# Optimization experiments

Measured on AMD Instinct MI355X. Metric: run time of the kernel, lower is better.

Reference implementation:

```python
import jax, jax.numpy as jnp
import numpy as np

B, F, SF = 2, 5, 15          # batch, query frames, num_shots*sframe
C, KD, VD = 1024, 128, 512   # encoder_dim, keydim, valdim
H = W = 32                   # l3 feature map (output stride 8 on 256x256)


def _conv(x, w, b, pad):
    y = jax.lax.conv_general_dilated(
        x, w, window_strides=(1, 1), padding=[(pad, pad), (pad, pad)],
        dimension_numbers=("NCHW", "OIHW", "NCHW"))
    return y + b[None, :, None, None]


def setup_inputs() -> dict:
    key = jax.random.key(0)
    ks = jax.random.split(key, 8)
    s = 0.02
    return {
        "query_feat": jax.random.normal(ks[0], (B * F, C, H, W), jnp.float32),
        "support_fg_feat": jax.random.normal(ks[1], (B * SF, C, H, W), jnp.float32),
        "w_sk": jax.random.normal(ks[2], (KD, C, 3, 3), jnp.float32) * s,
        "b_sk": jnp.zeros((KD,), jnp.float32),
        "w_sv": jax.random.normal(ks[3], (VD, C, 3, 3), jnp.float32) * s,
        "b_sv": jnp.zeros((VD,), jnp.float32),
        "w_qq": jax.random.normal(ks[4], (KD, C, 3, 3), jnp.float32) * s,
        "b_qq": jnp.zeros((KD,), jnp.float32),
        "w_qk": jax.random.normal(ks[5], (KD, C, 3, 3), jnp.float32) * s,
        "b_qk": jnp.zeros((KD,), jnp.float32),
        "w_cq": jax.random.normal(ks[6], (VD, C, 1, 1), jnp.float32) * s,
        "b_cq": jnp.zeros((VD,), jnp.float32),
    }


def reference(query_feat, support_fg_feat, w_sk, b_sk, w_sv, b_sv,
              w_qq, b_qq, w_qk, b_qk, w_cq, b_cq):
    hw = H * W
    # QKV projections (3x3 convs)
    sk = _conv(support_fg_feat, w_sk, b_sk, 1)   # [B*SF, KD, H, W]
    sv = _conv(support_fg_feat, w_sv, b_sv, 1)   # [B*SF, VD, H, W]
    qq = _conv(query_feat, w_qq, b_qq, 1)        # [B*F, KD, H, W]
    qk = _conv(query_feat, w_qk, b_qk, 1)        # [B*F, KD, H, W]

    # support K: [B, SF*hw, KD];  support V: [B, VD, SF*hw]
    support_k = sk.reshape(B, SF, KD, H, W).transpose(0, 2, 1, 3, 4)
    support_k = support_k.reshape(B, KD, SF * hw).transpose(0, 2, 1)
    support_v = sv.reshape(B, SF, VD, H, W).transpose(0, 2, 1, 3, 4)
    support_v = support_v.reshape(B, VD, SF * hw)

    qq5 = qq.reshape(B, F, KD, H, W)
    qk5 = qk.reshape(B, F, KD, H, W)
    mid = F // 2
    scale = 1.0 / jnp.sqrt(jnp.float32(KD))

    # stage 1: middle-frame query attends into support memory
    middle_q = qq5[:, mid].reshape(B, KD, hw)                 # [B, KD, hw]
    P1 = jnp.einsum("bkc,bcq->bkq", support_k, middle_q) * scale  # [B, SF*hw, hw]
    P1 = jax.nn.softmax(P1, axis=1)
    new_V = jnp.einsum("bvk,bkq->bvq", support_v, P1)          # [B, VD, hw]

    # stage 2: all-frame queries attend into middle-frame keys
    middle_K = qk5[:, mid].reshape(B, KD, hw).transpose(0, 2, 1)   # [B, hw, KD]
    qq_flat = qq5.transpose(0, 2, 1, 3, 4).reshape(B, KD, F * hw)  # [B, KD, F*hw]
    P2 = jnp.einsum("bkc,bcq->bkq", middle_K, qq_flat) * scale     # [B, hw, F*hw]
    P2 = jax.nn.softmax(P2, axis=1)
    Out = jnp.einsum("bvk,bkq->bvq", new_V, P2)                    # [B, VD, F*hw]

    after = Out.reshape(B, VD, F, H, W).transpose(0, 2, 1, 3, 4)
    after = after.reshape(B * F, VD, H, W)
    qf = _conv(query_feat, w_cq, b_cq, 0)                          # [B*F, VD, H, W]
    return jnp.concatenate([after, qf], axis=1)                    # [B*F, 2*VD, H, W]
```

## Files before the change

### kernel.cpp

```cpp
#include <hip/hip_runtime.h>
#include <cstdint>

typedef unsigned short u16;
typedef __attribute__((ext_vector_type(8))) u16 u16x8;
typedef __attribute__((ext_vector_type(4))) u16 u16x4;
typedef __attribute__((ext_vector_type(8))) _Float16 f16x8;
typedef __attribute__((ext_vector_type(4))) float f32x4;

__device__ __forceinline__ u16 f2h(float f) {
  _Float16 h = (_Float16)f;
  return __builtin_bit_cast(u16, h);
}
__device__ __forceinline__ float h2f(u16 b) {
  _Float16 h = __builtin_bit_cast(_Float16, b);
  return (float)h;
}
__device__ __forceinline__ void gll16(const void* g, void* l) {
  auto gp = reinterpret_cast<const __attribute__((address_space(1))) unsigned int*>(
      reinterpret_cast<uintptr_t>(g));
  auto lp = reinterpret_cast<__attribute__((address_space(3))) unsigned int*>(
      reinterpret_cast<uintptr_t>(l));
  __builtin_amdgcn_global_load_lds(gp, lp, 16, 0, 0);
}

__global__ __launch_bounds__(256) void pad_nhwc(const float* __restrict__ in,
                                                u16* __restrict__ outp) {
  const int img = blockIdx.x >> 5;
  const int y   = blockIdx.x & 31;
  __shared__ float tile[32][33];
  const int tid = threadIdx.x;
  u16* base = outp + (long)img * 34 * 34 * 1024;
  const u16x8 z8 = {0, 0, 0, 0, 0, 0, 0, 0};
  {
    u16* r = base + (long)(y + 1) * 34 * 1024;
    if (tid < 128) *(u16x8*)&r[tid * 8] = z8;
    else *(u16x8*)&r[33 * 1024 + (tid - 128) * 8] = z8;
  }
  if (y == 0) {
    for (int i = tid * 8; i < 34816; i += 2048) *(u16x8*)&base[i] = z8;
  }
  if (y == 31) {
    u16* r = base + 33L * 34 * 1024;
    for (int i = tid * 8; i < 34816; i += 2048) *(u16x8*)&r[i] = z8;
  }
  const int xi = tid & 31, ci = tid >> 5;
  const int xo = tid >> 3, q = tid & 7;
  const float* ip = in + (long)img * 1048576 + y * 32;
  u16* op = base + ((long)(y + 1) * 34 + 1) * 1024;
  for (int c0 = 0; c0 < 1024; c0 += 32) {
#pragma unroll
    for (int k2 = 0; k2 < 4; k2++)
      tile[k2 * 8 + ci][xi] = ip[(long)(c0 + k2 * 8 + ci) * 1024 + xi];
    __syncthreads();
    u16x4 o4;
#pragma unroll
    for (int r = 0; r < 4; r++) o4[r] = f2h(tile[q * 4 + r][xo]);
    *(u16x4*)&op[(long)xo * 1024 + c0 + q * 4] = o4;
    __syncthreads();
  }
}

__device__ __forceinline__ void wre3_body(const float* __restrict__ wp,
                                          u16* __restrict__ op, float* buf) {
  for (int i = threadIdx.x; i < 9216; i += 256) buf[i] = wp[i];
  __syncthreads();
  for (int k = threadIdx.x; k < 9216; k += 256) {
    const int cblk = k / 576;
    const int r = k - cblk * 576;
    const int t = r >> 6, ci = r & 63;
    op[k] = f2h(buf[(cblk * 64 + ci) * 9 + t]);
  }
}
__global__ __launch_bounds__(256) void wprep(
    const float* __restrict__ w_sk, const float* __restrict__ w_sv,
    const float* __restrict__ w_qq, const float* __restrict__ w_qk,
    const float* __restrict__ w_cq, u16* __restrict__ WTSK,
    u16* __restrict__ WTSV, u16* __restrict__ WTQQK, u16* __restrict__ WCQ) {
  __shared__ float buf[9216];
  const int b = blockIdx.x;
  if (b < 128) {
    wre3_body(w_sk + (long)b * 9216, WTSK + (long)b * 9216, buf);
  } else if (b < 640) {
    const int oc = b - 128;
    wre3_body(w_sv + (long)oc * 9216, WTSV + (long)oc * 9216, buf);
  } else if (b < 768) {
    const int oc = b - 640;
    wre3_body(w_qq + (long)oc * 9216, WTQQK + (long)oc * 9216, buf);
  } else if (b < 896) {
    const int oc = b - 768;
    wre3_body(w_qk + (long)oc * 9216, WTQQK + (long)(oc + 128) * 9216, buf);
  } else {
    const int i = (b - 896) * 1024 + threadIdx.x * 4;
#pragma unroll
    for (int r = 0; r < 4; r++) WCQ[i + r] = f2h(w_cq[i + r]);
  }
}

__global__ __launch_bounds__(256) void row_softmax60(u16* __restrict__ P) {
  u16* p = P + (long)blockIdx.x * 15360;
  const int tid = threadIdx.x;
  __shared__ float rm[4], rs[4];
  u16x4 v[15];
#pragma unroll
  for (int j = 0; j < 15; j++)
    v[j] = *(const u16x4*)(p + ((tid + (j << 8)) << 2));
  float m = -3.0e38f;
#pragma unroll
  for (int j = 0; j < 15; j++)
#pragma unroll
    for (int e = 0; e < 4; e++) m = fmaxf(m, h2f(v[j][e]));
#pragma unroll
  for (int o = 32; o > 0; o >>= 1) m = fmaxf(m, __shfl_xor(m, o, 64));
  if ((tid & 63) == 0) rm[tid >> 6] = m;
  __syncthreads();
  const float M = fmaxf(fmaxf(rm[0], rm[1]), fmaxf(rm[2], rm[3]));
  float s = 0.f;
#pragma unroll
  for (int j = 0; j < 15; j++)
#pragma unroll
    for (int e = 0; e < 4; e++) s += __expf(h2f(v[j][e]) - M);
#pragma unroll
  for (int o = 32; o > 0; o >>= 1) s += __shfl_xor(s, o, 64);
  if ((tid & 63) == 0) rs[tid >> 6] = s;
  __syncthreads();
  const float inv = 1.0f / (rs[0] + rs[1] + rs[2] + rs[3]);
#pragma unroll
  for (int j = 0; j < 15; j++) {
    u16x4 o4;
#pragma unroll
    for (int e = 0; e < 4; e++) o4[e] = f2h(__expf(h2f(v[j][e]) - M) * inv);
    *(u16x4*)(p + ((tid + (j << 8)) << 2)) = o4;
  }
}

__global__ __launch_bounds__(256) void row_softmax4(u16* __restrict__ P) {
  u16* p = P + (long)blockIdx.x * 1024;
  const int tid = threadIdx.x;
  __shared__ float rm[4], rs[4];
  u16x4 v = *(const u16x4*)(p + (tid << 2));
  float m = fmaxf(fmaxf(h2f(v[0]), h2f(v[1])), fmaxf(h2f(v[2]), h2f(v[3])));
#pragma unroll
  for (int o = 32; o > 0; o >>= 1) m = fmaxf(m, __shfl_xor(m, o, 64));
  if ((tid & 63) == 0) rm[tid >> 6] = m;
  __syncthreads();
  const float M = fmaxf(fmaxf(rm[0], rm[1]), fmaxf(rm[2], rm[3]));
  float s = 0.f;
#pragma unroll
  for (int e = 0; e < 4; e++) s += __expf(h2f(v[e]) - M);
#pragma unroll
  for (int o = 32; o > 0; o >>= 1) s += __shfl_xor(s, o, 64);
  if ((tid & 63) == 0) rs[tid >> 6] = s;
  __syncthreads();
  const float inv = 1.0f / (rs[0] + rs[1] + rs[2] + rs[3]);
  u16x4 o4;
#pragma unroll
  for (int e = 0; e < 4; e++) o4[e] = f2h(__expf(h2f(v[e]) - M) * inv);
  *(u16x4*)(p + (tid << 2)) = o4;
}

__global__ __launch_bounds__(256) void reduce8h(const u16* __restrict__ part,
                                                u16* __restrict__ o) {
  long j = ((long)blockIdx.x * 256 + threadIdx.x) * 4;
  int b = (int)(j >> 19);
  long i = j & 524287;
  const u16* p = part + (long)b * 4194304 + i;
  float s0 = 0.f, s1 = 0.f, s2 = 0.f, s3 = 0.f;
#pragma unroll
  for (int c = 0; c < 8; c++) {
    u16x4 v = *(const u16x4*)&p[(long)c * 524288];
    s0 += h2f(v[0]); s1 += h2f(v[1]); s2 += h2f(v[2]); s3 += h2f(v[3]);
  }
  u16x4 o4 = {f2h(s0), f2h(s1), f2h(s2), f2h(s3)};
  *(u16x4*)&o[j] = o4;
}
__global__ __launch_bounds__(256) void reduce_sk(const float* __restrict__ part,
                                                 const float* __restrict__ bias,
                                                 u16* __restrict__ o) {
  long i = ((long)blockIdx.x * 256 + threadIdx.x) * 4;
  f32x4 s = *(const f32x4*)&part[i];
  s = s + *(const f32x4*)&part[i + 3932160];
  f32x4 bb = *(const f32x4*)&bias[(int)(i & 127)];
  u16x4 o4;
#pragma unroll
  for (int r = 0; r < 4; r++) o4[r] = f2h(s[r] + bb[r]);
  *(u16x4*)&o[i] = o4;
}
__global__ __launch_bounds__(256) void reduce_qqk(
    const float* __restrict__ part, const float* __restrict__ b_qq,
    const float* __restrict__ b_qk, u16* __restrict__ QQR,
    u16* __restrict__ QKR) {
  long i = ((long)blockIdx.x * 256 + threadIdx.x) * 4;
  const int n = (int)(i >> 8), m = (int)(i & 255);
  f32x4 s = *(const f32x4*)&part[i];
  s = s + *(const f32x4*)&part[i + 2621440];
  const int lo = (m < 128);
  const int mm = m & 127;
  const float* bs = lo ? b_qq : b_qk;
  f32x4 bb = *(const f32x4*)&bs[mm];
  u16* dst = (lo ? QQR : QKR) + (long)n * 128 + mm;
  u16x4 o4;
#pragma unroll
  for (int r = 0; r < 4; r++) o4[r] = f2h(s[r] + bb[r]);
  *(u16x4*)dst = o4;
}

__global__ __launch_bounds__(512, 1)
void gemm256(const u16* __restrict__ A, const u16* __restrict__ B,
             const float* __restrict__ bias, u16* __restrict__ out) {
  __shared__ u16 lds[81920];
  const int tid = threadIdx.x, lane = tid & 63, wave = tid >> 6;
  const int nwg = gridDim.x * gridDim.y;
  int wg = blockIdx.x + gridDim.x * blockIdx.y;
  wg = (wg & 7) * (nwg >> 3) + (wg >> 3);
  const int ntile = wg % gridDim.x;
  const int mtile = wg / gridDim.x;

  const int slog = (lane & 7) ^ ((lane >> 3) & 7);
  const u16* aS[4];
  const u16* bS[4];
  int aD[4], bD[4];
#pragma unroll
  for (int j = 0; j < 4; j++) {
    const int r = wave * 32 + j * 8 + (lane >> 3);
    aS[j] = A + (long)(mtile * 256 + r) * 9216 + slog * 8;
    aD[j] = (wave * 32 + j * 8) * 64;
    const int n = ntile * 256 + r;
    const int img = n >> 10, p = n & 1023;
    const int y = p >> 5, x = p & 31;
    bS[j] = B + ((long)((img * 34 + y) * 34 + x)) * 1024 + slog * 8;
    bD[j] = (wave * 32 + j * 8) * 64;
  }

  const int g = lane >> 4, l15 = lane & 15;
  const int wm = wave >> 2, wn = wave & 3;
  int aRow[8], bRow[4], sx[2];
#pragma unroll
  for (int mi = 0; mi < 8; mi++) aRow[mi] = (wm * 128 + mi * 16 + l15) * 64;
#pragma unroll
  for (int ni = 0; ni < 4; ni++) bRow[ni] = (wn * 64 + ni * 16 + l15) * 64;
#pragma unroll
  for (int ks = 0; ks < 2; ks++) sx[ks] = ((ks * 4 + g) ^ (l15 & 7)) * 8;

  auto conv_badd = [](int kt) {
    const int cblk = kt / 9;
    const int t = kt - cblk * 9;
    const int dy = t / 3, dx = t - dy * 3;
    return (dy * 34 + dx) * 1024 + cblk * 64;
  };

  f32x4 acc[8][4];
  const f32x4 zero = {0.f, 0.f, 0.f, 0.f};
#pragma unroll
  for (int i = 0; i < 8; i++)
#pragma unroll
    for (int j = 0; j < 4; j++) acc[i][j] = zero;

  const int nkt = 144;
  {
#pragma unroll
    for (int j = 0; j < 4; j++) gll16(aS[j], &lds[aD[j]]);
    const int b0 = conv_badd(0), b1 = conv_badd(1);
#pragma unroll
    for (int j = 0; j < 4; j++) gll16(bS[j] + b0, &lds[32768 + bD[j]]);
#pragma unroll
    for (int j = 0; j < 4; j++) gll16(bS[j] + b1, &lds[49152 + bD[j]]);
    asm volatile("s_waitcnt vmcnt(4)" ::: "memory");
    __builtin_amdgcn_s_barrier();
  }

  int bc = 0;
  for (int kt = 0; kt < nkt; ++kt) {
    const int abuf = (kt & 1) << 14;
    const int anbuf = abuf ^ 16384;
    const int bbuf = 32768 + bc * 16384;
    int bsn = bc + 2; if (bsn >= 3) bsn -= 3;
    const int bnbuf = 32768 + bsn * 16384;
    const bool stA = (kt + 1 < nkt);
    const bool stB = (kt + 2 < nkt);
    const int kA = (kt + 1) << 6;
    const int bAdd2 = stB ? conv_badd(kt + 2) : 0;
    f16x8 afr[4], bfr[4];
#pragma unroll
    for (int mi = 0; mi < 4; mi++) afr[mi] = *(const f16x8*)&lds[abuf + aRow[mi] + sx[0]];
#pragma unroll
    for (int ni = 0; ni < 4; ni++) bfr[ni] = *(const f16x8*)&lds[bbuf + bRow[ni] + sx[0]];
    if (stA) {
      gll16(aS[0] + kA, &lds[anbuf + aD[0]]);
      gll16(aS[1] + kA, &lds[anbuf + aD[1]]);
    }
    __builtin_amdgcn_s_barrier();
    __builtin_amdgcn_s_setprio(1);
#pragma unroll
    for (int mi = 0; mi < 4; mi++)
#pragma unroll
      for (int ni = 0; ni < 4; ni++)
        acc[mi][ni] = __builtin_amdgcn_mfma_f32_16x16x32_f16(afr[mi], bfr[ni], acc[mi][ni], 0, 0, 0);
    __builtin_amdgcn_s_setprio(0);
    __builtin_amdgcn_s_barrier();
#pragma unroll
    for (int mi = 0; mi < 4; mi++) afr[mi] = *(const f16x8*)&lds[abuf + aRow[mi + 4] + sx[0]];
    if (stA) {
      gll16(aS[2] + kA, &lds[anbuf + aD[2]]);
      gll16(aS[3] + kA, &lds[anbuf + aD[3]]);
    }
    __builtin_amdgcn_s_barrier();
    __builtin_amdgcn_s_setprio(1);
#pragma unroll
    for (int mi = 0; mi < 4; mi++)
#pragma unroll
      for (int ni = 0; ni < 4; ni++)
        acc[mi + 4][ni] = __builtin_amdgcn_mfma_f32_16x16x32_f16(afr[mi], bfr[ni], acc[mi + 4][ni], 0, 0, 0);
    __builtin_amdgcn_s_setprio(0);
    __builtin_amdgcn_s_barrier();
#pragma unroll
    for (int mi = 0; mi < 4; mi++) afr[mi] = *(const f16x8*)&lds[abuf + aRow[mi] + sx[1]];
#pragma unroll
    for (int ni = 0; ni < 4; ni++) bfr[ni] = *(const f16x8*)&lds[bbuf + bRow[ni] + sx[1]];
    if (stB) {
      gll16(bS[0] + bAdd2, &lds[bnbuf + bD[0]]);
      gll16(bS[1] + bAdd2, &lds[bnbuf + bD[1]]);
    }
    __builtin_amdgcn_s_barrier();
    __builtin_amdgcn_s_setprio(1);
#pragma unroll
    for (int mi = 0; mi < 4; mi++)
#pragma unroll
      for (int ni = 0; ni < 4; ni++)
        acc[mi][ni] = __builtin_amdgcn_mfma_f32_16x16x32_f16(afr[mi], bfr[ni], acc[mi][ni], 0, 0, 0);
    __builtin_amdgcn_s_setprio(0);
    __builtin_amdgcn_s_barrier();
#pragma unroll
    for (int mi = 0; mi < 4; mi++) afr[mi] = *(const f16x8*)&lds[abuf + aRow[mi + 4] + sx[1]];
    if (stB) {
      gll16(bS[2] + bAdd2, &lds[bnbuf + bD[2]]);
      gll16(bS[3] + bAdd2, &lds[bnbuf + bD[3]]);
    }
    __builtin_amdgcn_s_barrier();
    __builtin_amdgcn_s_setprio(1);
#pragma unroll
    for (int mi = 0; mi < 4; mi++)
#pragma unroll
      for (int ni = 0; ni < 4; ni++)
        acc[mi + 4][ni] = __builtin_amdgcn_mfma_f32_16x16x32_f16(afr[mi], bfr[ni], acc[mi + 4][ni], 0, 0, 0);
    __builtin_amdgcn_s_setprio(0);
    if (stB) {
      asm volatile("s_waitcnt vmcnt(4)" ::: "memory");
    } else if (stA) {
      asm volatile("s_waitcnt vmcnt(0)" ::: "memory");
    }
    __builtin_amdgcn_s_barrier();
    bc = bc + 1; if (bc >= 3) bc -= 3;
  }

#pragma unroll
  for (int mi = 0; mi < 8; mi++) {
#pragma unroll
    for (int ni = 0; ni < 4; ni++) {
      f32x4 v = acc[mi][ni];
      const int m0 = mtile * 256 + wm * 128 + mi * 16 + g * 4;
      const int n = ntile * 256 + wn * 64 + ni * 16 + l15;
      const int b = (n >= 15360) ? 1 : 0;
      const int rem = n - b * 15360;
#pragma unroll
      for (int r = 0; r < 4; r++) {
        const int m = m0 + r;
        out[(long)b * 7864320 + (long)m * 15360 + rem] = f2h(v[r] + bias[m]);
      }
    }
  }
}

template <int BMODE, int EPI, int SPLITK>
__global__ __launch_bounds__(256, 2)
void gemm_nt(const u16* __restrict__ A, long Azoff, int Astride,
             const u16* __restrict__ B, long Bzoff, int Bstride,
             int K, float scale,
             const float* __restrict__ bias, const float* __restrict__ bias2,
             void* __restrict__ out0, void* __restrict__ out1,
             long out_zoff, int ldo) {
  __shared__ u16 lds[4 * 8192];
  const int tid = threadIdx.x;
  const int lane = tid & 63;
  const int wave = tid >> 6;
  const int mtile = blockIdx.y, ntile = blockIdx.x, z = blockIdx.z;

  const int zb = (SPLITK > 1) ? z / SPLITK : z;
  const int zc = (SPLITK > 1) ? z % SPLITK : 0;
  const u16* Ab = A + (long)zb * Azoff + (long)zc * K;
  const u16* Bb = B + (long)zb * Bzoff + ((BMODE == 0) ? (long)zc * K : 0);

  const int r8 = lane >> 3;
  const int sphys = lane & 7;
  const u16* aSrc[4];
  const u16* bSrc[4];
  u16* aDst[4];
  u16* bDst[4];
#pragma unroll
  for (int i = 0; i < 4; i++) {
    const int row = wave * 32 + i * 8 + r8;
    const int slog = sphys ^ (row & 7);
    aSrc[i] = Ab + (long)(mtile * 128 + row) * Astride + slog * 8;
    if (BMODE == 0) {
      bSrc[i] = Bb + (long)(ntile * 128 + row) * Bstride + slog * 8;
    } else {
      const int n = ntile * 128 + row;
      const int img = n >> 10;
      const int p = n & 1023;
      const int y = p >> 5, x = p & 31;
      bSrc[i] = Bb + ((long)(img * 34 + y) * 34 + x) * 1024 + slog * 8;
    }
    aDst[i] = &lds[0] + (wave * 32 + i * 8) * 64;
    bDst[i] = &lds[0] + 8192 + (wave * 32 + i * 8) * 64;
  }

  const int g = lane >> 4, l15 = lane & 15;
  const int wm = wave >> 1, wn = wave & 1;
  int offA[2][4], offB[2][4];
#pragma unroll
  for (int ks = 0; ks < 2; ks++) {
    const int sl = ks * 4 + g;
#pragma unroll
    for (int i = 0; i < 4; i++) {
      const int ra = wm * 64 + i * 16 + l15;
      offA[ks][i] = ra * 64 + ((sl ^ (ra & 7)) * 8);
      const int rb = wn * 64 + i * 16 + l15;
      offB[ks][i] = 8192 + rb * 64 + ((sl ^ (rb & 7)) * 8);
    }
  }

  auto stage = [&](int buf, int kb) {
    int bAdd;
    if (BMODE == 0) {
      bAdd = kb;
    } else if (BMODE == 1) {
      const int ktg = (zc * K + kb) >> 6;
      const int cblk = ktg / 9;
      const int t = ktg - cblk * 9;
      const int dy = t / 3, dx = t - dy * 3;
      bAdd = (dy * 34 + dx) * 1024 + cblk * 64;
    } else {
      bAdd = 35 * 1024 + kb;
    }
    const int bufo = buf * 16384;
#pragma unroll
    for (int i = 0; i < 4; i++) gll16(aSrc[i] + kb, aDst[i] + bufo);
#pragma unroll
    for (int i = 0; i < 4; i++) gll16(bSrc[i] + bAdd, bDst[i] + bufo);
  };

  f32x4 acc[4][4];
  const f32x4 zero = {0.f, 0.f, 0.f, 0.f};
#pragma unroll
  for (int i = 0; i < 4; i++)
#pragma unroll
    for (int j = 0; j < 4; j++) acc[i][j] = zero;

  const int nkt = K >> 6;
  stage(0, 0);
  __syncthreads();
  for (int kt = 0; kt < nkt; ++kt) {
    const int buf = kt & 1;
    if (kt + 1 < nkt) stage(buf ^ 1, (kt + 1) << 6);
#pragma unroll
    for (int ks = 0; ks < 2; ks++) {
      f16x8 af[4], bfg[4];
#pragma unroll
      for (int i = 0; i < 4; i++)
        af[i] = *(const f16x8*)&lds[buf * 16384 + offA[ks][i]];
#pragma unroll
      for (int i = 0; i < 4; i++)
        bfg[i] = *(const f16x8*)&lds[buf * 16384 + offB[ks][i]];
#pragma unroll
      for (int mi = 0; mi < 4; mi++)
#pragma unroll
        for (int ni = 0; ni < 4; ni++)
          acc[mi][ni] = __builtin_amdgcn_mfma_f32_16x16x32_f16(
              af[mi], bfg[ni], acc[mi][ni], 0, 0, 0);
    }
    __syncthreads();
  }

#pragma unroll
  for (int mi = 0; mi < 4; mi++) {
#pragma unroll
    for (int ni = 0; ni < 4; ni++) {
      f32x4 v = acc[mi][ni];
      const int m0 = mtile * 128 + wm * 64 + mi * 16 + g * 4;
      const int n = ntile * 128 + wn * 64 + ni * 16 + l15;
      if (EPI == 0) {
        u16* ob = (u16*)out0;
        const float* bs = bias;
        int mm = m0;
        if (out1 != nullptr && m0 >= 128) { ob = (u16*)out1; bs = bias2; mm = m0 - 128; }
        u16x4 pk;
#pragma unroll
        for (int r = 0; r < 4; r++) {
          float val = v[r] * scale + (bs ? bs[mm + r] : 0.f);
          pk[r] = f2h(val);
        }
        *(u16x4*)&ob[(long)n * ldo + mm] = pk;
      } else if (EPI == 1) {
        u16* ob = (u16*)out0 + (long)z * out_zoff;
#pragma unroll
        for (int r = 0; r < 4; r++) {
          const int m = m0 + r;
          float val = v[r] * scale + (bias ? bias[m] : 0.f);
          ob[(long)m * ldo + n] = f2h(val);
        }
      } else if (EPI == 2) {
        float* of = (float*)out0;
        const int img = n >> 10, p = n & 1023;
#pragma unroll
        for (int r = 0; r < 4; r++) {
          const int m = m0 + r;
          of[(long)img * 1048576 + (long)(512 + m) * 1024 + p] =
              v[r] + (bias ? bias[m] : 0.f);
        }
      } else if (EPI == 3) {
        float* of = (float*)out0;
        const int f = n >> 10, p = n & 1023;
#pragma unroll
        for (int r = 0; r < 4; r++) {
          const int m = m0 + r;
          of[(long)z * 5242880 + (long)f * 1048576 + (long)m * 1024 + p] = v[r];
        }
      } else if (EPI == 4) {
        float* of = (float*)out0 + (long)z * out_zoff;
#pragma unroll
        for (int r = 0; r < 4; r++) of[(long)(m0 + r) * ldo + n] = v[r];
      } else if (EPI == 5) {
        float* of = (float*)out0 + (long)zc * out_zoff;
        *(f32x4*)&of[(long)n * ldo + m0] = v;
      } else {
        u16* ob = (u16*)out0 + (long)z * out_zoff;
#pragma unroll
        for (int r = 0; r < 4; r++) ob[(long)(m0 + r) * ldo + n] = f2h(v[r]);
      }
    }
  }
}

extern "C" void kernel_launch(void* const* d_in, const int* in_sizes, int n_in,
                              void* d_out, int out_size, void* d_ws, size_t ws_size,
                              hipStream_t stream) {
  (void)in_sizes; (void)n_in; (void)out_size;
  const float* query   = (const float*)d_in[0];
  const float* support = (const float*)d_in[1];
  const float* w_sk = (const float*)d_in[2];  const float* b_sk = (const float*)d_in[3];
  const float* w_sv = (const float*)d_in[4];  const float* b_sv = (const float*)d_in[5];
  const float* w_qq = (const float*)d_in[6];  const float* b_qq = (const float*)d_in[7];
  const float* w_qk = (const float*)d_in[8];  const float* b_qk = (const float*)d_in[9];
  const float* w_cq = (const float*)d_in[10]; const float* b_cq = (const float*)d_in[11];
  float* out = (float*)d_out;
  char* ws = (char*)d_ws;

  if (ws_size < 158924800u) return;

  u16* PQ    = (u16*)(ws + 0);
  u16* PS    = (u16*)(ws + 23674880);
  u16* WTSK  = (u16*)(ws + 94699520);
  u16* WTSV  = (u16*)(ws + 97058816);
  u16* WTQQK = (u16*)(ws + 106496000);
  u16* WCQ   = (u16*)(ws + 111214592);
  u16* SKR   = (u16*)(ws + 112263168);
  u16* SVA   = (u16*)(ws + 120127488);
  u16* QQR   = (u16*)(ws + 151584768);
  u16* QKR   = (u16*)(ws + 154206208);
  u16* NEWV  = (u16*)(ws + 156827648);
  u16* P1T   = PS;
  u16* P2T   = PQ;
  u16* PART2 = (u16*)(ws + 94699520);
  float* PARTK = (float*)SVA;
  float* PARTQ = (float*)SVA;

  const float SCALE = 0.08838834764831843f;

  pad_nhwc<<<dim3(320), 256, 0, stream>>>(query, PQ);
  pad_nhwc<<<dim3(960), 256, 0, stream>>>(support, PS);
  wprep<<<dim3(1408), 256, 0, stream>>>(w_sk, w_sv, w_qq, w_qk, w_cq,
                                        WTSK, WTSV, WTQQK, WCQ);

  gemm_nt<1, 5, 2><<<dim3(240, 1, 2), 256, 0, stream>>>(
      WTSK, 0, 9216, PS, 0, 0, 4608, 1.0f, nullptr, nullptr, PARTK, nullptr,
      3932160L, 128);
  reduce_sk<<<dim3(3840), 256, 0, stream>>>(PARTK, b_sk, SKR);

  gemm_nt<1, 5, 2><<<dim3(80, 2, 2), 256, 0, stream>>>(
      WTQQK, 0, 9216, PQ, 0, 0, 4608, 1.0f, nullptr, nullptr, PARTQ, nullptr,
      2621440L, 256);
  reduce_qqk<<<dim3(2560), 256, 0, stream>>>(PARTQ, b_qq, b_qk, QQR, QKR);

  gemm256<<<dim3(120, 2), 512, 0, stream>>>(WTSV, PS, b_sv, SVA);

  gemm_nt<2, 2, 1><<<dim3(80, 4, 1), 256, 0, stream>>>(
      WCQ, 0, 1024, PQ, 0, 0, 1024, 1.0f, b_cq, nullptr, out, nullptr, 0, 0);

  gemm_nt<0, 1, 1><<<dim3(120, 8, 2), 256, 0, stream>>>(
      QQR + 262144, 655360L, 128, SKR, 1966080L, 128, 128, SCALE, nullptr,
      nullptr, P1T, nullptr, 15728640L, 15360);
  row_softmax60<<<dim3(2048), 256, 0, stream>>>(P1T);
  gemm_nt<0, 6, 8><<<dim3(8, 4, 16), 256, 0, stream>>>(
      SVA, 7864320L, 15360, P1T, 15728640L, 15360, 1920, 1.0f, nullptr,
      nullptr, PART2, nullptr, 524288L, 1024);
  reduce8h<<<dim3(1024), 256, 0, stream>>>(PART2, NEWV);

  gemm_nt<0, 1, 1><<<dim3(8, 40, 2), 256, 0, stream>>>(
      QQR, 655360L, 128, QKR + 262144, 655360L, 128, 128, SCALE, nullptr,
      nullptr, P2T, nullptr, 5242880L, 1024);
  row_softmax4<<<dim3(10240), 256, 0, stream>>>(P2T);
  gemm_nt<0, 3, 1><<<dim3(40, 4, 2), 256, 0, stream>>>(
      NEWV, 524288L, 1024, P2T, 5242880L, 1024, 1024, 1.0f, nullptr, nullptr,
      out, nullptr, 0, 0);
}
```

Baseline: 668.8 us.

## Software-pipeline conv GEMM fragments across iterations and drop intra-iteration barriers

```diff
diff --git a/kernel.cpp b/kernel.cpp
--- a/kernel.cpp
+++ b/kernel.cpp
@@ -204,7 +204,7 @@
   *(u16x4*)dst = o4;
 }
 
-__global__ __launch_bounds__(512, 1)
+__global__ __launch_bounds__(512, 2)
 void gemm256(const u16* __restrict__ A, const u16* __restrict__ B,
              const float* __restrict__ bias, u16* __restrict__ out) {
   __shared__ u16 lds[81920];
@@ -259,14 +259,21 @@
   {
 #pragma unroll
     for (int j = 0; j < 4; j++) gll16(aS[j], &lds[aD[j]]);
-    const int b0 = conv_badd(0), b1 = conv_badd(1);
-#pragma unroll
-    for (int j = 0; j < 4; j++) gll16(bS[j] + b0, &lds[32768 + bD[j]]);
-#pragma unroll
-    for (int j = 0; j < 4; j++) gll16(bS[j] + b1, &lds[49152 + bD[j]]);
+    const int b0o = conv_badd(0), b1o = conv_badd(1);
+#pragma unroll
+    for (int j = 0; j < 4; j++) gll16(bS[j] + b0o, &lds[32768 + bD[j]]);
+#pragma unroll
+    for (int j = 0; j < 4; j++) gll16(bS[j] + b1o, &lds[49152 + bD[j]]);
     asm volatile("s_waitcnt vmcnt(4)" ::: "memory");
     __builtin_amdgcn_s_barrier();
   }
+
+  f16x8 a0[4], a1[4], a3[4], b0[4], b2[4];
+  f16x8 zf;
+#pragma unroll
+  for (int j = 0; j < 8; j++) zf[j] = (_Float16)0.0f;
+#pragma unroll
+  for (int i = 0; i < 4; i++) { a3[i] = zf; b2[i] = zf; }
 
   int bc = 0;
   for (int kt = 0; kt < nkt; ++kt) {
@@ -279,70 +286,51 @@
     const bool stB = (kt + 2 < nkt);
     const int kA = (kt + 1) << 6;
     const int bAdd2 = stB ? conv_badd(kt + 2) : 0;
-    f16x8 afr[4], bfr[4];
-#pragma unroll
-    for (int mi = 0; mi < 4; mi++) afr[mi] = *(const f16x8*)&lds[abuf + aRow[mi] + sx[0]];
-#pragma unroll
-    for (int ni = 0; ni < 4; ni++) bfr[ni] = *(const f16x8*)&lds[bbuf + bRow[ni] + sx[0]];
+
+#pragma unroll
+    for (int i = 0; i < 4; i++) a0[i] = *(const f16x8*)&lds[abuf + aRow[i] + sx[0]];
+#pragma unroll
+    for (int i = 0; i < 4; i++) b0[i] = *(const f16x8*)&lds[bbuf + bRow[i] + sx[0]];
+#pragma unroll
+    for (int i = 0; i < 4; i++) a1[i] = *(const f16x8*)&lds[abuf + aRow[i + 4] + sx[0]];
+#pragma unroll
+    for (int mi = 0; mi < 4; mi++)
+#pragma unroll
+      for (int ni = 0; ni < 4; ni++)
+        acc[mi + 4][ni] = __builtin_amdgcn_mfma_f32_16x16x32_f16(
+            a3[mi], b2[ni], acc[mi + 4][ni], 0, 0, 0);
     if (stA) {
-      gll16(aS[0] + kA, &lds[anbuf + aD[0]]);
-      gll16(aS[1] + kA, &lds[anbuf + aD[1]]);
-    }
-    __builtin_amdgcn_s_barrier();
-    __builtin_amdgcn_s_setprio(1);
+#pragma unroll
+      for (int j = 0; j < 4; j++) gll16(aS[j] + kA, &lds[anbuf + aD[j]]);
+    }
 #pragma unroll
     for (int mi = 0; mi < 4; mi++)
 #pragma unroll
       for (int ni = 0; ni < 4; ni++)
-        acc[mi][ni] = __builtin_amdgcn_mfma_f32_16x16x32_f16(afr[mi], bfr[ni], acc[mi][ni], 0, 0, 0);
-    __builtin_amdgcn_s_setprio(0);
-    __builtin_amdgcn_s_barrier();
-#pragma unroll
-    for (int mi = 0; mi < 4; mi++) afr[mi] = *(const f16x8*)&lds[abuf + aRow[mi + 4] + sx[0]];
-    if (stA) {
-      gll16(aS[2] + kA, &lds[anbuf + aD[2]]);
-      gll16(aS[3] + kA, &lds[anbuf + aD[3]]);
-    }
-    __builtin_amdgcn_s_barrier();
-    __builtin_amdgcn_s_setprio(1);
+        acc[mi][ni] = __builtin_amdgcn_mfma_f32_16x16x32_f16(
+            a0[mi], b0[ni], acc[mi][ni], 0, 0, 0);
+#pragma unroll
+    for (int i = 0; i < 4; i++) a0[i] = *(const f16x8*)&lds[abuf + aRow[i] + sx[1]];
+#pragma unroll
+    for (int i = 0; i < 4; i++) b2[i] = *(const f16x8*)&lds[bbuf + bRow[i] + sx[1]];
+    if (stB) {
+#pragma unroll
+      for (int j = 0; j < 4; j++) gll16(bS[j] + bAdd2, &lds[bnbuf + bD[j]]);
+    }
 #pragma unroll
     for (int mi = 0; mi < 4; mi++)
 #pragma unroll
       for (int ni = 0; ni < 4; ni++)
-        acc[mi + 4][ni] = __builtin_amdgcn_mfma_f32_16x16x32_f16(afr[mi], bfr[ni], acc[mi + 4][ni], 0, 0, 0);
-    __builtin_amdgcn_s_setprio(0);
-    __builtin_amdgcn_s_barrier();
-#pragma unroll
-    for (int mi = 0; mi < 4; mi++) afr[mi] = *(const f16x8*)&lds[abuf + aRow[mi] + sx[1]];
-#pragma unroll
-    for (int ni = 0; ni < 4; ni++) bfr[ni] = *(const f16x8*)&lds[bbuf + bRow[ni] + sx[1]];
-    if (stB) {
-      gll16(bS[0] + bAdd2, &lds[bnbuf + bD[0]]);
-      gll16(bS[1] + bAdd2, &lds[bnbuf + bD[1]]);
-    }
-    __builtin_amdgcn_s_barrier();
-    __builtin_amdgcn_s_setprio(1);
+        acc[mi + 4][ni] = __builtin_amdgcn_mfma_f32_16x16x32_f16(
+            a1[mi], b0[ni], acc[mi + 4][ni], 0, 0, 0);
+#pragma unroll
+    for (int i = 0; i < 4; i++) a3[i] = *(const f16x8*)&lds[abuf + aRow[i + 4] + sx[1]];
 #pragma unroll
     for (int mi = 0; mi < 4; mi++)
 #pragma unroll
       for (int ni = 0; ni < 4; ni++)
-        acc[mi][ni] = __builtin_amdgcn_mfma_f32_16x16x32_f16(afr[mi], bfr[ni], acc[mi][ni], 0, 0, 0);
-    __builtin_amdgcn_s_setprio(0);
-    __builtin_amdgcn_s_barrier();
-#pragma unroll
-    for (int mi = 0; mi < 4; mi++) afr[mi] = *(const f16x8*)&lds[abuf + aRow[mi + 4] + sx[1]];
-    if (stB) {
-      gll16(bS[2] + bAdd2, &lds[bnbuf + bD[2]]);
-      gll16(bS[3] + bAdd2, &lds[bnbuf + bD[3]]);
-    }
-    __builtin_amdgcn_s_barrier();
-    __builtin_amdgcn_s_setprio(1);
-#pragma unroll
-    for (int mi = 0; mi < 4; mi++)
-#pragma unroll
-      for (int ni = 0; ni < 4; ni++)
-        acc[mi + 4][ni] = __builtin_amdgcn_mfma_f32_16x16x32_f16(afr[mi], bfr[ni], acc[mi + 4][ni], 0, 0, 0);
-    __builtin_amdgcn_s_setprio(0);
+        acc[mi][ni] = __builtin_amdgcn_mfma_f32_16x16x32_f16(
+            a0[mi], b2[ni], acc[mi][ni], 0, 0, 0);
     if (stB) {
       asm volatile("s_waitcnt vmcnt(4)" ::: "memory");
     } else if (stA) {
@@ -351,6 +339,12 @@
     __builtin_amdgcn_s_barrier();
     bc = bc + 1; if (bc >= 3) bc -= 3;
   }
+#pragma unroll
+  for (int mi = 0; mi < 4; mi++)
+#pragma unroll
+    for (int ni = 0; ni < 4; ni++)
+      acc[mi + 4][ni] = __builtin_amdgcn_mfma_f32_16x16x32_f16(
+          a3[mi], b2[ni], acc[mi + 4][ni], 0, 0, 0);
 
 #pragma unroll
   for (int mi = 0; mi < 8; mi++) {
```

Result: no change. 659.6 us (-1.4%).
